# Kernel tuning notes

Measured on AMD Instinct MI355X. Metric: run time of the kernel, lower is better.

Reference implementation:

```python
import jax, jax.numpy as jnp
import numpy as np

B, S, H, NH = 8, 2048, 256, 4
D = H // NH
EPS = 1e-12


def setup_inputs() -> dict:
    key = jax.random.key(0)
    ks = jax.random.split(key, 8)
    w = lambda k: jax.random.normal(k, (H, H), jnp.float32) * 0.02
    return {
        "input_tensor": jax.random.normal(ks[0], (B, S, H), jnp.float32),
        "attribute_table": jax.random.normal(ks[1], (B, S, 1, H), jnp.float32),
        "position_embedding": jax.random.normal(ks[2], (B, S, H), jnp.float32),
        "attention_mask": jnp.zeros((B, 1, S, S), jnp.float32),
        "Wq": w(ks[3]), "bq": jnp.zeros((H,), jnp.float32),
        "Wk": w(ks[4]), "bk": jnp.zeros((H,), jnp.float32),
        "Wv": w(ks[5]), "bv": jnp.zeros((H,), jnp.float32),
        "Wd": w(ks[6]), "bd": jnp.zeros((H,), jnp.float32),
        "gamma": jnp.ones((H,), jnp.float32),
        "beta": jnp.zeros((H,), jnp.float32),
    }


def _layer_norm(x, g, b):
    mu = jnp.mean(x, axis=-1, keepdims=True)
    var = jnp.mean(jnp.square(x - mu), axis=-1, keepdims=True)
    return (x - mu) * jax.lax.rsqrt(var + EPS) * g + b


def reference(input_tensor, attribute_table, position_embedding, attention_mask,
              Wq, bq, Wk, bk, Wv, bv, Wd, bd, gamma, beta):
    # fusion_type == 'sum': sum attribute tables + item emb + position emb
    mixed = jnp.sum(attribute_table, axis=-2) + input_tensor + position_embedding  # [B,S,H]
    q = (mixed @ Wq + bq).reshape(B, S, NH, D)
    k = (mixed @ Wk + bk).reshape(B, S, NH, D)
    v = (input_tensor @ Wv + bv).reshape(B, S, NH, D)  # value from raw item emb
    scores = jnp.einsum('bqhd,bkhd->bhqk', q, k) / jnp.sqrt(jnp.float32(D))
    scores = scores + attention_mask  # additive mask broadcast over heads
    probs = jax.nn.softmax(scores, axis=-1)  # attn_dropout p=0 (eval)
    ctx = jnp.einsum('bhqk,bkhd->bqhd', probs, v).reshape(B, S, H)
    hidden = ctx @ Wd + bd  # out_dropout p=0 (eval)
    return _layer_norm(hidden + input_tensor, gamma, beta)
```

## Files before the change

kernel.cpp:

```cpp
#include <hip/hip_runtime.h>
#include <hip/hip_bf16.h>
#include <math.h>

#define BB 8
#define SS 2048
#define HH 256
#define NHH 4
#define DD 64
#define MROWS (BB*SS)

typedef unsigned short u16;
typedef unsigned int   u32;
typedef __attribute__((ext_vector_type(8))) short bf16x8;
typedef __attribute__((ext_vector_type(4))) float f32x4;
typedef __attribute__((ext_vector_type(8))) u16   u16x8;
typedef __attribute__((ext_vector_type(4))) u16   u16x4;

__device__ inline u16 f2bf(float f) {
    union { float f; u32 u; } v; v.f = f;
    u32 r = v.u + 0x7fffu + ((v.u >> 16) & 1u);
    return (u16)(r >> 16);
}
__device__ inline float bf2f(u16 h) {
    union { u32 u; float f; } v; v.u = (u32)h << 16; return v.f;
}
__device__ inline void gload16(const u16* g, u16* l) {
    __builtin_amdgcn_global_load_lds(
        (const __attribute__((address_space(1))) u32*)g,
        (__attribute__((address_space(3))) u32*)l, 16, 0, 0);
}

__global__ __launch_bounds__(256) void fuse_mixed_cast(const float* __restrict__ inp,
    const float* __restrict__ attr, const float* __restrict__ pos,
    u16* __restrict__ mixed, u16* __restrict__ inpb, int n8) {
    int i = blockIdx.x * 256 + threadIdx.x;
    if (i >= n8) return;
    const f32x4* pi = (const f32x4*)(inp  + (size_t)i*8);
    const f32x4* pa = (const f32x4*)(attr + (size_t)i*8);
    const f32x4* pp = (const f32x4*)(pos  + (size_t)i*8);
    u16x8 om, oi;
    #pragma unroll
    for (int h = 0; h < 2; ++h) {
        f32x4 a = pi[h], b = pa[h], c = pp[h];
        #pragma unroll
        for (int j = 0; j < 4; ++j) {
            om[h*4+j] = f2bf(a[j] + b[j] + c[j]);
            oi[h*4+j] = f2bf(a[j]);
        }
    }
    *(u16x8*)(mixed + (size_t)i*8) = om;
    *(u16x8*)(inpb  + (size_t)i*8) = oi;
}

__global__ __launch_bounds__(256) void transpose_w(const float* __restrict__ W0,
    const float* __restrict__ W1, const float* __restrict__ W2,
    const float* __restrict__ W3, u16* __restrict__ Wt) {
    const float* W = blockIdx.y==0 ? W0 : blockIdx.y==1 ? W1 : blockIdx.y==2 ? W2 : W3;
    u16* dst = Wt + (size_t)blockIdx.y*65536;
    int kt = blockIdx.x & 3, nt = blockIdx.x >> 2;
    __shared__ float T[64][65];
    int tid = threadIdx.x;
    int r = tid >> 2, cq = tid & 3;
    const float* src = W + (size_t)(kt*64 + r)*HH + nt*64 + cq*16;
    #pragma unroll
    for (int j = 0; j < 4; ++j) {
        f32x4 v = ((const f32x4*)src)[j];
        T[r][cq*16 + j*4 + 0] = v[0];
        T[r][cq*16 + j*4 + 1] = v[1];
        T[r][cq*16 + j*4 + 2] = v[2];
        T[r][cq*16 + j*4 + 3] = v[3];
    }
    __syncthreads();
    u16x8 o0, o1;
    #pragma unroll
    for (int j = 0; j < 8; ++j) o0[j] = f2bf(T[cq*16 + j][r]);
    #pragma unroll
    for (int j = 0; j < 8; ++j) o1[j] = f2bf(T[cq*16 + 8 + j][r]);
    u16* d = dst + (size_t)(nt*64 + r)*HH + kt*64 + cq*16;
    *(u16x8*)d       = o0;
    *(u16x8*)(d + 8) = o1;
}

template<bool VT>
__global__ __launch_bounds__(256) void gemm_mfma(
    const u16* __restrict__ A0, const u16* __restrict__ A1,
    const u16* __restrict__ Wt, const float* __restrict__ bias0,
    const float* __restrict__ bias1, u16* __restrict__ O0, u16* __restrict__ O1)
{
    __shared__ u16 As[2][128*64];
    __shared__ u16 Ws[2][128*64];
    int tid = threadIdx.x;
    int w = tid >> 6, l = tid & 63;
    int lq = l & 15, g4 = l >> 4;
    int w0 = w >> 1, w1 = w & 1;
    int z = blockIdx.z;
    const u16* A = z ? A1 : A0;
    const u16* Wz = Wt + (size_t)z*65536;
    const float* bias = z ? bias1 : bias0;
    u16* Oz = z ? O1 : O0;
    int bm = blockIdx.x*128, bn = blockIdx.y*128;

    int rr0 = l >> 3;
    int cc0 = (l & 7) ^ (rr0 & 7);
    const u16* agp[4]; const u16* wgp[4];
    #pragma unroll
    for (int q = 0; q < 4; ++q) {
        int rr = (w*4+q)*8 + rr0;
        agp[q] = A  + (size_t)(bm + rr)*HH + cc0*8;
        wgp[q] = Wz + (size_t)(bn + rr)*HH + cc0*8;
    }

    f32x4 acc[4][4];
    #pragma unroll
    for (int i = 0; i < 4; ++i)
        #pragma unroll
        for (int j = 0; j < 4; ++j) acc[i][j] = (f32x4){0.f,0.f,0.f,0.f};

    #define STAGE(buf, k0) { \
        _Pragma("unroll") \
        for (int q = 0; q < 4; ++q) { \
            gload16(agp[q] + (k0), &As[buf][(w*4+q)*512]); \
            gload16(wgp[q] + (k0), &Ws[buf][(w*4+q)*512]); \
        } }

    STAGE(0, 0);
    __syncthreads();
    int cur = 0;
    #pragma unroll
    for (int t = 0; t < 4; ++t) {
        if (t < 3) STAGE(cur^1, (t+1)*64);
        #pragma unroll
        for (int kk = 0; kk < 2; ++kk) {
            bf16x8 af[4], wf[4];
            #pragma unroll
            for (int i = 0; i < 4; ++i) {
                int row = w0*64 + i*16 + lq;
                int cc = (kk*4 + g4) ^ (row & 7);
                af[i] = *(const bf16x8*)&As[cur][row*64 + cc*8];
            }
            #pragma unroll
            for (int j = 0; j < 4; ++j) {
                int row = w1*64 + j*16 + lq;
                int cc = (kk*4 + g4) ^ (row & 7);
                wf[j] = *(const bf16x8*)&Ws[cur][row*64 + cc*8];
            }
            #pragma unroll
            for (int i = 0; i < 4; ++i)
                #pragma unroll
                for (int j = 0; j < 4; ++j) {
                    if (VT)
                        acc[i][j] = __builtin_amdgcn_mfma_f32_16x16x32_bf16(af[i], wf[j], acc[i][j], 0,0,0);
                    else
                        acc[i][j] = __builtin_amdgcn_mfma_f32_16x16x32_bf16(wf[j], af[i], acc[i][j], 0,0,0);
                }
        }
        __syncthreads();
        cur ^= 1;
    }

    if (!VT) {
        #pragma unroll
        for (int i = 0; i < 4; ++i) {
            size_t m = bm + w0*64 + i*16 + lq;
            #pragma unroll
            for (int j = 0; j < 4; ++j) {
                int n = bn + w1*64 + j*16 + g4*4;
                f32x4 bb = *(const f32x4*)&bias[n];
                u16x4 o;
                #pragma unroll
                for (int r = 0; r < 4; ++r) o[r] = f2bf(acc[i][j][r] + bb[r]);
                *(u16x4*)&Oz[m*HH + n] = o;
            }
        }
    } else {
        int b = bm >> 11;
        int sb = bm & 2047;
        #pragma unroll
        for (int i = 0; i < 4; ++i) {
            int s = sb + w0*64 + i*16 + g4*4;
            #pragma unroll
            for (int j = 0; j < 4; ++j) {
                int n = bn + w1*64 + j*16 + lq;
                float bs = bias[n];
                int h = n >> 6, d = n & 63;
                u16x4 o;
                #pragma unroll
                for (int r = 0; r < 4; ++r) o[r] = f2bf(acc[i][j][r] + bs);
                *(u16x4*)&Oz[(((size_t)b*NHH + h)*DD + d)*SS + s] = o;
            }
        }
    }
    #undef STAGE
}

__global__ __launch_bounds__(512) void attn_mfma(
    const u16* __restrict__ Qb, const u16* __restrict__ Kb,
    const u16* __restrict__ Vt, const float* __restrict__ mask,
    u16* __restrict__ O)
{
    __shared__ u16 KT[2][64*64];
    __shared__ u16 VTs[2][64*64];
    __shared__ u16 PT[8][16*64];

    int tid = threadIdx.x;
    int w = tid >> 6, l = tid & 63;
    int lq = l & 15, g = l >> 4;
    int qb = blockIdx.x, h = blockIdx.y, b = blockIdx.z;
    int q = qb*128 + w*16 + lq;

    bf16x8 qf[2];
    {
        const u16* qp = Qb + ((size_t)(b*SS + q))*HH + h*DD + g*8;
        qf[0] = *(const bf16x8*)qp;
        qf[1] = *(const bf16x8*)(qp + 32);
    }

    int srow = tid >> 3;
    int sch  = tid & 7;
    const u16* kgp = Kb + ((size_t)(b*SS + srow))*HH + h*DD + sch*8;
    const u16* vgp = Vt + (((size_t)(b*NHH + h))*DD + srow)*SS + sch*8;
    int sidx = srow*64 + ((sch ^ (srow & 7)))*8;

    const float* mrow = mask + ((size_t)b*SS + q)*SS + g*4;

    f32x4 ot[4];
    #pragma unroll
    for (int dt = 0; dt < 4; ++dt) ot[dt] = (f32x4){0.f,0.f,0.f,0.f};
    float m = -1e30f, lsum = 0.f;

    u16x8 kr = *(const u16x8*)kgp;
    u16x8 vr = *(const u16x8*)vgp;
    f32x4 mra[4], mrb[4];
    #pragma unroll
    for (int kt = 0; kt < 4; ++kt) mra[kt] = *(const f32x4*)(mrow + kt*16);
    *(u16x8*)&KT[0][sidx]  = kr;
    *(u16x8*)&VTs[0][sidx] = vr;
    __syncthreads();

    for (int t = 0; t < SS/64; ++t) {
        int cur = t & 1;
        if (t < SS/64 - 1) {
            kr = *(const u16x8*)(kgp + (size_t)(t+1)*64*HH);
            vr = *(const u16x8*)(vgp + (t+1)*64);
            #pragma unroll
            for (int kt = 0; kt < 4; ++kt)
                mrb[kt] = *(const f32x4*)(mrow + (t+1)*64 + kt*16);
        }

        f32x4 st[4];
        #pragma unroll
        for (int kt = 0; kt < 4; ++kt) {
            st[kt] = (f32x4){0.f,0.f,0.f,0.f};
            int key = kt*16 + lq;
            #pragma unroll
            for (int df = 0; df < 2; ++df) {
                int c = (4*df + g) ^ (key & 7);
                bf16x8 a = *(const bf16x8*)&KT[cur][key*64 + c*8];
                st[kt] = __builtin_amdgcn_mfma_f32_16x16x32_bf16(a, qf[df], st[kt], 0,0,0);
            }
        }

        float p[4][4];
        float tm = -1e30f;
        #pragma unroll
        for (int kt = 0; kt < 4; ++kt)
            #pragma unroll
            for (int j = 0; j < 4; ++j) {
                float s = st[kt][j]*0.125f + mra[kt][j];
                p[kt][j] = s;
                tm = fmaxf(tm, s);
            }
        tm = fmaxf(tm, __shfl_xor(tm, 16));
        tm = fmaxf(tm, __shfl_xor(tm, 32));
        float mn = fmaxf(m, tm);
        float scale = __expf(m - mn);
        float rs = 0.f;
        #pragma unroll
        for (int kt = 0; kt < 4; ++kt)
            #pragma unroll
            for (int j = 0; j < 4; ++j) {
                float e = __expf(p[kt][j] - mn);
                p[kt][j] = e;
                rs += e;
            }
        rs += __shfl_xor(rs, 16);
        rs += __shfl_xor(rs, 32);
        lsum = lsum*scale + rs;
        m = mn;
        #pragma unroll
        for (int dt = 0; dt < 4; ++dt) {
            ot[dt][0] *= scale; ot[dt][1] *= scale;
            ot[dt][2] *= scale; ot[dt][3] *= scale;
        }

        #pragma unroll
        for (int kt = 0; kt < 4; ++kt) {
            u16x4 pk;
            pk[0] = f2bf(p[kt][0]); pk[1] = f2bf(p[kt][1]);
            pk[2] = f2bf(p[kt][2]); pk[3] = f2bf(p[kt][3]);
            int koff = kt*16 + g*4;
            int c = (koff >> 3) ^ (lq & 7);
            int idx = lq*64 + c*8 + (koff & 7);
            *(u16x4*)&PT[w][idx] = pk;
        }

        bf16x8 pb[2];
        #pragma unroll
        for (int kt2 = 0; kt2 < 2; ++kt2) {
            int c = (4*kt2 + g) ^ (lq & 7);
            pb[kt2] = *(const bf16x8*)&PT[w][lq*64 + c*8];
        }
        #pragma unroll
        for (int dt = 0; dt < 4; ++dt) {
            int d = dt*16 + lq;
            #pragma unroll
            for (int kt2 = 0; kt2 < 2; ++kt2) {
                int c = (4*kt2 + g) ^ (d & 7);
                bf16x8 a = *(const bf16x8*)&VTs[cur][d*64 + c*8];
                ot[dt] = __builtin_amdgcn_mfma_f32_16x16x32_bf16(a, pb[kt2], ot[dt], 0,0,0);
            }
        }

        if (t < SS/64 - 1) {
            *(u16x8*)&KT[cur^1][sidx]  = kr;
            *(u16x8*)&VTs[cur^1][sidx] = vr;
            #pragma unroll
            for (int kt = 0; kt < 4; ++kt) mra[kt] = mrb[kt];
        }
        __syncthreads();
    }

    float inv = 1.0f / lsum;
    #pragma unroll
    for (int dt = 0; dt < 4; ++dt) {
        u16x4 o;
        #pragma unroll
        for (int j = 0; j < 4; ++j) o[j] = f2bf(ot[dt][j] * inv);
        *(u16x4*)&O[((size_t)(b*SS + q))*HH + h*DD + dt*16 + g*4] = o;
    }
}

__global__ __launch_bounds__(256) void add_ln(const u16* __restrict__ hidden,
    const float* __restrict__ inp, const float* __restrict__ gamma,
    const float* __restrict__ beta, float* __restrict__ out) {
    int row = blockIdx.x;
    int tid = threadIdx.x;
    int lane = tid & 63, wave = tid >> 6;
    __shared__ float red[8];
    float x = bf2f(hidden[(size_t)row*HH + tid]) + inp[(size_t)row*HH + tid];
    float s = x;
    #pragma unroll
    for (int o = 32; o; o >>= 1) s += __shfl_xor(s, o);
    if (!lane) red[wave] = s;
    __syncthreads();
    float mu = (red[0] + red[1] + red[2] + red[3]) * (1.0f/HH);
    float dx = x - mu;
    float v = dx * dx;
    #pragma unroll
    for (int o = 32; o; o >>= 1) v += __shfl_xor(v, o);
    if (!lane) red[4 + wave] = v;
    __syncthreads();
    float var = (red[4] + red[5] + red[6] + red[7]) * (1.0f/HH);
    out[(size_t)row*HH + tid] = dx * rsqrtf(var + 1e-12f) * gamma[tid] + beta[tid];
}

extern "C" void kernel_launch(void* const* d_in, const int* in_sizes, int n_in,
                              void* d_out, int out_size, void* d_ws, size_t ws_size,
                              hipStream_t stream) {
    const float* inp   = (const float*)d_in[0];
    const float* attr  = (const float*)d_in[1];
    const float* pos   = (const float*)d_in[2];
    const float* mask  = (const float*)d_in[3];
    const float* Wq    = (const float*)d_in[4];
    const float* bq    = (const float*)d_in[5];
    const float* Wk    = (const float*)d_in[6];
    const float* bk    = (const float*)d_in[7];
    const float* Wv    = (const float*)d_in[8];
    const float* bv    = (const float*)d_in[9];
    const float* Wd    = (const float*)d_in[10];
    const float* bd    = (const float*)d_in[11];
    const float* gamma = (const float*)d_in[12];
    const float* beta  = (const float*)d_in[13];
    float* out = (float*)d_out;

    const size_t NEL = (size_t)BB*SS*HH;
    u16* mixed = (u16*)d_ws;
    u16* inpb  = mixed + NEL;
    u16* Qb    = mixed + 2*NEL;
    u16* Kb    = mixed + 3*NEL;
    u16* Vtb   = mixed + 4*NEL;
    u16* ctx   = mixed + 5*NEL;
    u16* hid   = mixed + 6*NEL;
    u16* Wt    = mixed + 7*NEL;

    fuse_mixed_cast<<<(int)(NEL/8/256), 256, 0, stream>>>(inp, attr, pos, mixed, inpb, (int)(NEL/8));
    transpose_w<<<dim3(16,4), 256, 0, stream>>>(Wq, Wk, Wv, Wd, Wt);

    gemm_mfma<false><<<dim3(128,2,2), 256, 0, stream>>>(mixed, mixed, Wt, bq, bk, Qb, Kb);
    gemm_mfma<true ><<<dim3(128,2,1), 256, 0, stream>>>(inpb, inpb, Wt + 2*65536, bv, bv, Vtb, Vtb);

    attn_mfma<<<dim3(SS/128, NHH, BB), 512, 0, stream>>>(Qb, Kb, Vtb, mask, ctx);

    gemm_mfma<false><<<dim3(128,2,1), 256, 0, stream>>>(ctx, ctx, Wt + 3*65536, bd, bd, hid, hid);

    add_ln<<<MROWS, 256, 0, stream>>>(hid, inp, gamma, beta, out);
}
```

Baseline: 136.7 us.

## Lazy softmax rescale, exp2 math, setprio around MFMAs, bf16 residual in LN

Reworks the attention inner loop: scores become exp2 with a folded log2e, the running-max rescale is skipped while the new max stays within a threshold of the old one, the reductions are tree-shaped, and s_setprio is raised around the MFMA blocks. The loop is unrolled by 2 and bf16 conversion uses the library intrinsic. The add+LayerNorm kernel now reads the bf16 copy of the input instead of fp32, halving that read traffic. The bf16 residual lowers accuracy of the final output slightly.

```diff
diff --git a/kernel.cpp b/kernel.cpp
--- a/kernel.cpp
+++ b/kernel.cpp
@@ -8,6 +8,7 @@
 #define NHH 4
 #define DD 64
 #define MROWS (BB*SS)
+#define LOG2E 1.44269504f
 
 typedef unsigned short u16;
 typedef unsigned int   u32;
@@ -21,8 +22,19 @@
     u32 r = v.u + 0x7fffu + ((v.u >> 16) & 1u);
     return (u16)(r >> 16);
 }
+__device__ inline u16 f2bf_n(float f) {
+    __hip_bfloat16 h = __float2bfloat16(f);
+    return *(u16*)&h;
+}
 __device__ inline float bf2f(u16 h) {
     union { u32 u; float f; } v; v.u = (u32)h << 16; return v.f;
+}
+__device__ inline float fexp2(float x) {
+#if __has_builtin(__builtin_amdgcn_exp2f)
+    return __builtin_amdgcn_exp2f(x);
+#else
+    return __expf(x * 0.6931471806f);
+#endif
 }
 __device__ inline void gload16(const u16* g, u16* l) {
     __builtin_amdgcn_global_load_lds(
@@ -237,6 +249,7 @@
     *(u16x8*)&VTs[0][sidx] = vr;
     __syncthreads();
 
+    #pragma unroll 2
     for (int t = 0; t < SS/64; ++t) {
         int cur = t & 1;
         if (t < SS/64 - 1) {
@@ -248,6 +261,7 @@
         }
 
         f32x4 st[4];
+        __builtin_amdgcn_s_setprio(1);
         #pragma unroll
         for (int kt = 0; kt < 4; ++kt) {
             st[kt] = (f32x4){0.f,0.f,0.f,0.f};
@@ -259,45 +273,56 @@
                 st[kt] = __builtin_amdgcn_mfma_f32_16x16x32_bf16(a, qf[df], st[kt], 0,0,0);
             }
         }
-
-        float p[4][4];
-        float tm = -1e30f;
+        __builtin_amdgcn_s_setprio(0);
+
+        float s[4][4];
         #pragma unroll
         for (int kt = 0; kt < 4; ++kt)
             #pragma unroll
-            for (int j = 0; j < 4; ++j) {
-                float s = st[kt][j]*0.125f + mra[kt][j];
-                p[kt][j] = s;
-                tm = fmaxf(tm, s);
-            }
+            for (int j = 0; j < 4; ++j)
+                s[kt][j] = __builtin_fmaf(st[kt][j], 0.125f, mra[kt][j]);
+
+        float cm[4];
+        #pragma unroll
+        for (int kt = 0; kt < 4; ++kt)
+            cm[kt] = fmaxf(fmaxf(s[kt][0], s[kt][1]), fmaxf(s[kt][2], s[kt][3]));
+        float tm = fmaxf(fmaxf(cm[0], cm[1]), fmaxf(cm[2], cm[3]));
         tm = fmaxf(tm, __shfl_xor(tm, 16));
         tm = fmaxf(tm, __shfl_xor(tm, 32));
-        float mn = fmaxf(m, tm);
-        float scale = __expf(m - mn);
-        float rs = 0.f;
+
+        if (!__all(tm <= m + 8.0f)) {
+            float mn = fmaxf(m, tm);
+            float sc = fexp2((m - mn) * LOG2E);
+            lsum *= sc;
+            #pragma unroll
+            for (int dt = 0; dt < 4; ++dt) {
+                ot[dt][0] *= sc; ot[dt][1] *= sc;
+                ot[dt][2] *= sc; ot[dt][3] *= sc;
+            }
+            m = mn;
+        }
+        float mnl = m * LOG2E;
+
+        float e[4][4];
         #pragma unroll
         for (int kt = 0; kt < 4; ++kt)
             #pragma unroll
-            for (int j = 0; j < 4; ++j) {
-                float e = __expf(p[kt][j] - mn);
-                p[kt][j] = e;
-                rs += e;
-            }
+            for (int j = 0; j < 4; ++j)
+                e[kt][j] = fexp2(__builtin_fmaf(s[kt][j], LOG2E, -mnl));
+        float cs[4];
+        #pragma unroll
+        for (int kt = 0; kt < 4; ++kt)
+            cs[kt] = (e[kt][0] + e[kt][1]) + (e[kt][2] + e[kt][3]);
+        float rs = (cs[0] + cs[1]) + (cs[2] + cs[3]);
         rs += __shfl_xor(rs, 16);
         rs += __shfl_xor(rs, 32);
-        lsum = lsum*scale + rs;
-        m = mn;
-        #pragma unroll
-        for (int dt = 0; dt < 4; ++dt) {
-            ot[dt][0] *= scale; ot[dt][1] *= scale;
-            ot[dt][2] *= scale; ot[dt][3] *= scale;
-        }
+        lsum += rs;
 
         #pragma unroll
         for (int kt = 0; kt < 4; ++kt) {
             u16x4 pk;
-            pk[0] = f2bf(p[kt][0]); pk[1] = f2bf(p[kt][1]);
-            pk[2] = f2bf(p[kt][2]); pk[3] = f2bf(p[kt][3]);
+            #pragma unroll
+            for (int j = 0; j < 4; ++j) pk[j] = f2bf_n(e[kt][j]);
             int koff = kt*16 + g*4;
             int c = (koff >> 3) ^ (lq & 7);
             int idx = lq*64 + c*8 + (koff & 7);
@@ -310,6 +335,7 @@
             int c = (4*kt2 + g) ^ (lq & 7);
             pb[kt2] = *(const bf16x8*)&PT[w][lq*64 + c*8];
         }
+        __builtin_amdgcn_s_setprio(1);
         #pragma unroll
         for (int dt = 0; dt < 4; ++dt) {
             int d = dt*16 + lq;
@@ -320,6 +346,7 @@
                 ot[dt] = __builtin_amdgcn_mfma_f32_16x16x32_bf16(a, pb[kt2], ot[dt], 0,0,0);
             }
         }
+        __builtin_amdgcn_s_setprio(0);
 
         if (t < SS/64 - 1) {
             *(u16x8*)&KT[cur^1][sidx]  = kr;
@@ -335,19 +362,19 @@
     for (int dt = 0; dt < 4; ++dt) {
         u16x4 o;
         #pragma unroll
-        for (int j = 0; j < 4; ++j) o[j] = f2bf(ot[dt][j] * inv);
+        for (int j = 0; j < 4; ++j) o[j] = f2bf_n(ot[dt][j] * inv);
         *(u16x4*)&O[((size_t)(b*SS + q))*HH + h*DD + dt*16 + g*4] = o;
     }
 }
 
 __global__ __launch_bounds__(256) void add_ln(const u16* __restrict__ hidden,
-    const float* __restrict__ inp, const float* __restrict__ gamma,
+    const u16* __restrict__ inpb, const float* __restrict__ gamma,
     const float* __restrict__ beta, float* __restrict__ out) {
     int row = blockIdx.x;
     int tid = threadIdx.x;
     int lane = tid & 63, wave = tid >> 6;
     __shared__ float red[8];
-    float x = bf2f(hidden[(size_t)row*HH + tid]) + inp[(size_t)row*HH + tid];
+    float x = bf2f(hidden[(size_t)row*HH + tid]) + bf2f(inpb[(size_t)row*HH + tid]);
     float s = x;
     #pragma unroll
     for (int o = 32; o; o >>= 1) s += __shfl_xor(s, o);
@@ -403,5 +430,5 @@
 
     gemm_mfma<false><<<dim3(128,2,1), 256, 0, stream>>>(ctx, ctx, Wt + 3*65536, bd, bd, hid, hid);
 
-    add_ln<<<MROWS, 256, 0, stream>>>(hid, inp, gamma, beta, out);
-}
+    add_ln<<<MROWS, 256, 0, stream>>>(hid, inpb, gamma, beta, out);
+}
```

Result: slower. 139.7 us (+2.2%).
